# Kernel tuning notes

Measured on AMD Instinct MI355X. Metric: run time of the kernel, lower is better.

Reference implementation:

```python
import jax, jax.numpy as jnp
import numpy as np

N_NODES = 100_000
N_EDGES = 1_000_000
H = 128
NUM_STATES = 4
UPPER_T, LOWER_T, NUM_ITERS, TEMP_EVAL = 1.0, 0.1, 10000, 0.1


def temp_by_step(step, upper, lower, num_iters, temp_eval):
    # Python-level schedule: eval temp at step == -1, else linear anneal.
    if step == -1:
        return temp_eval
    frac = min(step / num_iters, 1.0)
    return upper + (lower - upper) * frac


def from_binary_states(states):
    # [*, k] bits -> integer id in [0, 2**k)
    weights = 2 ** jnp.arange(states.shape[-1])
    return (states * weights).sum(-1)


def setup_inputs() -> dict:
    key = jax.random.key(0)
    ks = jax.random.split(key, 20)
    N, E, h = N_NODES, N_EDGES, H
    node_states = jax.random.randint(ks[0], (N, NUM_STATES), 0, 2)
    edge_states = jax.random.randint(ks[1], (E, NUM_STATES), 0, 2)
    scalars = jax.random.normal(ks[2], (E, 1), jnp.float32)
    # first N edges are self-loops ordered by node id (required by the module's
    # node_scalars = scalars[src == dst] indexing convention)
    loops = jnp.arange(N)
    src = jax.random.randint(ks[3], (E - N,), 0, N)
    dst = jax.random.randint(ks[4], (E - N,), 0, N)
    dst = jnp.where(dst == src, (dst + 1) % N, dst)  # no accidental self-loops
    edge_index = jnp.stack([jnp.concatenate([loops, src]),
                            jnp.concatenate([loops, dst])])
    batched_reverse_idx = jax.random.randint(ks[5], (E,), 0, E)
    batch_scalars = jax.random.normal(ks[6], (E, 1, 1), jnp.float32)
    s = 0.02
    params = dict(
        node_emb=s * jax.random.normal(ks[7], (2 ** NUM_STATES, h), jnp.float32),
        edge_emb=s * jax.random.normal(ks[8], (2 ** NUM_STATES, h), jnp.float32),
        combine_W=s * jax.random.normal(ks[9], (2 * h, h), jnp.float32),
        combine_b=jnp.zeros((h,), jnp.float32),
        keep_W=s * jax.random.normal(ks[10], (h, 2), jnp.float32),
        keep_b=jnp.zeros((2,), jnp.float32),
        push_W=s * jax.random.normal(ks[11], (h, 2), jnp.float32),
        push_b=jnp.zeros((2,), jnp.float32),
        push_node_W=s * jax.random.normal(ks[12], (h, 2), jnp.float32),
        push_node_b=jnp.zeros((2,), jnp.float32),
        increment_W=s * jax.random.normal(ks[13], (h, 2), jnp.float32),
        increment_b=jnp.zeros((2,), jnp.float32),
    )
    return dict(node_states=node_states, edge_states=edge_states, scalars=scalars,
                edge_index=edge_index, batched_reverse_idx=batched_reverse_idx,
                batch_scalars=batch_scalars, processor_step=0, training_step=0,
                **params)


def reference(node_states, edge_states, scalars, edge_index, batched_reverse_idx,
              batch_scalars, processor_step, training_step,
              node_emb, edge_emb, combine_W, combine_b, keep_W, keep_b,
              push_W, push_b, push_node_W, push_node_b,
              increment_W, increment_b):
    N = node_states.shape[0]
    tau = temp_by_step(int(training_step), UPPER_T, LOWER_T, NUM_ITERS, TEMP_EVAL)
    # use_noise = config.use_noise (False) and training_step != -1 -> False

    node_fts = node_emb[from_binary_states(node_states)]   # [N, h]
    edge_fts = edge_emb[from_binary_states(edge_states)]   # [E, h]
    src, dst = edge_index[0], edge_index[1]
    fts = jnp.concatenate([edge_fts[batched_reverse_idx], node_fts[src]], axis=1)
    fts = fts @ combine_W + combine_b                       # [E, h]

    s = scalars.reshape(-1)                                 # [E]

    def pair_gumbel_first(W, b):
        # grouped (per-edge pair) softmax; take first component (== [::2])
        logits = (fts @ W + b) / tau                        # [E, 2]
        return jax.nn.softmax(logits, axis=-1)[:, 0]

    increment = 1.0 * pair_gumbel_first(increment_W, increment_b)
    keep = s * pair_gumbel_first(keep_W, keep_b)

    # push: first N edges are self-loops, self-loop of node i is edge i
    push_wo = pair_gumbel_first(push_W, push_b)
    push_w = pair_gumbel_first(push_node_W, push_node_b)
    node_scalars = s[:N]                                    # scalars at self-loops
    s_wo = s - node_scalars[dst]
    s_w = s_wo + node_scalars[src]
    acc = (jax.ops.segment_sum(push_wo * s_wo, dst, num_segments=N)
           + jax.ops.segment_sum(push_w * s_w, dst, num_segments=N))  # [N]
    edge_push = jnp.zeros_like(s).at[:N].set(acc)           # nonzero only on self-loops

    new_scalars = (increment + keep + edge_push)[:, None]   # [E, 1]
    target = batch_scalars[:, processor_step]               # [E, 1]
    loss = jnp.mean((target - new_scalars) ** 2)
    return new_scalars, loss
```

## Files before the change

### kernel.cpp

```cpp
#include <hip/hip_runtime.h>
#include <math.h>
#include <stdint.h>

#define N_NODES 100000
#define N_EDGES 1000000
#define N_NONLOOP (N_EDGES - N_NODES)
#define NXCD 8

typedef float  vfloat4 __attribute__((ext_vector_type(4)));
typedef int    vint4   __attribute__((ext_vector_type(4)));

#define XCC_ID_HWREG (20 | ((4 - 1) << 11))

__device__ __forceinline__ int get_xcc() {
    return __builtin_amdgcn_s_getreg(XCC_ID_HWREG) & (NXCD - 1);
}

__device__ __forceinline__ void l2_atomic_add(float* p, float v) {
    asm volatile("global_atomic_add_f32 %0, %1, off" :: "v"(p), "v"(v) : "memory");
}

__device__ __forceinline__ float get_invtau(const int* __restrict__ training_step) {
    int step = training_step[0];
    float tau;
    if (step == -1) {
        tau = 0.1f;
    } else {
        float frac = fminf((float)step / 10000.0f, 1.0f);
        tau = 1.0f + (0.1f - 1.0f) * frac;
    }
    return 1.0f / tau;
}

__device__ __forceinline__ float wave_reduce(float v) {
    #pragma unroll
    for (int off = 32; off > 0; off >>= 1) v += __shfl_down(v, off, 64);
    return v;
}

#define TAB_BLOCKS  132
#define NODE_BLOCKS 391
#define EI_BLOCKS   977

__global__ __launch_bounds__(256) void fused_pre(
    const int* __restrict__ node_states,
    const float* __restrict__ s,
    const int* __restrict__ edge_states,
    const int* __restrict__ brev,
    const float* __restrict__ node_emb,
    const float* __restrict__ edge_emb,
    const float* __restrict__ cW, const float* __restrict__ cb,
    const float* __restrict__ kW, const float* __restrict__ kb,
    const float* __restrict__ pW, const float* __restrict__ pb,
    const float* __restrict__ pnW, const float* __restrict__ pnb,
    const float* __restrict__ iW, const float* __restrict__ ib,
    const int* __restrict__ tstep,
    float2* __restrict__ node_pack,
    float* __restrict__ acc,
    uint8_t* __restrict__ ei,
    uint8_t* __restrict__ eib_node,
    float* __restrict__ tabs,
    float* __restrict__ lossp,
    float* __restrict__ loss_out,
    int ncopies)
{
    const int b = blockIdx.x;

    if (b < TAB_BLOCKS) {
        const int w    = b;
        const int lane = threadIdx.x & 63;
        const int wv   = threadIdx.x >> 6;
        const float invtau = get_invtau(tstep);
        __shared__ float part[4];

        float p = 0.f;
        if (w < 128) {
            const int isB = w >> 6, h = (w >> 4) & 3, i = w & 15;
            const float* emb = isB ? node_emb : edge_emb;
            const float* cWh = cW + isB * 128 * 128;
            float t0 = 0.f, t1 = 0.f;
            const int l0 = wv * 32;
            #pragma unroll 8
            for (int l = l0; l < l0 + 32; ++l) {
                const float el = emb[i * 128 + l];
                t0 += el * cWh[l * 128 + lane];
                t1 += el * cWh[l * 128 + 64 + lane];
            }
            const float* W = (h == 0) ? kW : (h == 1) ? pW : (h == 2) ? pnW : iW;
            const float wd0 = W[2 * lane] - W[2 * lane + 1];
            const float wd1 = W[2 * (lane + 64)] - W[2 * (lane + 64) + 1];
            p = t0 * wd0 + t1 * wd1;
        } else if (wv == 0) {
            const int h = w & 3;
            const float* W = (h == 0) ? kW : (h == 1) ? pW : (h == 2) ? pnW : iW;
            const float wd0 = W[2 * lane] - W[2 * lane + 1];
            const float wd1 = W[2 * (lane + 64)] - W[2 * (lane + 64) + 1];
            p = cb[lane] * wd0 + cb[64 + lane] * wd1;
        }
        p = wave_reduce(p);
        if (lane == 0) part[wv] = p;
        __syncthreads();
        if (threadIdx.x == 0) {
            const float tot = part[0] + part[1] + part[2] + part[3];
            if (w < 128) {
                const int isB = w >> 6, h = (w >> 4) & 3, i = w & 15;
                tabs[isB * 64 + i * 4 + h] = tot * invtau;
            } else {
                const int h = w & 3;
                const float* bb = (h == 0) ? kb : (h == 1) ? pb : (h == 2) ? pnb : ib;
                tabs[128 + h] = (tot + bb[0] - bb[1]) * invtau;
            }
        }
        return;
    }

    if (b < TAB_BLOCKS + NODE_BLOCKS) {
        const int n = (b - TAB_BLOCKS) * 256 + threadIdx.x;
        if (n < 256) lossp[n] = 0.f;
        if (n == 0) *loss_out = 0.f;
        if (n < N_NODES) {
            vint4 st = __builtin_nontemporal_load(&((const vint4*)node_states)[n]);
            const int idx = st.x + 2 * st.y + 4 * st.z + 8 * st.w;
            float2 np;
            np.x = s[n];
            np.y = __int_as_float(idx);
            node_pack[n] = np;
            for (int k = 0; k < ncopies; ++k) acc[(size_t)k * N_NODES + n] = 0.f;
            const int rev = brev[n];
            const int4 est = ((const int4*)edge_states)[rev];
            eib_node[n] = (uint8_t)(est.x + 2 * est.y + 4 * est.z + 8 * est.w);
        }
        return;
    }

    const int t = (b - TAB_BLOCKS - NODE_BLOCKS) * 256 + threadIdx.x;
    if (t < N_EDGES / 4) {
        const vint4* esp = (const vint4*)edge_states + 4 * t;
        vint4 e0 = __builtin_nontemporal_load(esp + 0);
        vint4 e1 = __builtin_nontemporal_load(esp + 1);
        vint4 e2 = __builtin_nontemporal_load(esp + 2);
        vint4 e3 = __builtin_nontemporal_load(esp + 3);
        const uint32_t i0 = e0.x + 2 * e0.y + 4 * e0.z + 8 * e0.w;
        const uint32_t i1 = e1.x + 2 * e1.y + 4 * e1.z + 8 * e1.w;
        const uint32_t i2 = e2.x + 2 * e2.y + 4 * e2.z + 8 * e2.w;
        const uint32_t i3 = e3.x + 2 * e3.y + 4 * e3.z + 8 * e3.w;
        ((uint32_t*)ei)[t] = i0 | (i1 << 8) | (i2 << 16) | (i3 << 24);
    }
}

template<int MODE>
__global__ __launch_bounds__(256) void edge_kernel(
    const float* __restrict__ s,
    const int* __restrict__ src,
    const int* __restrict__ dst,
    const int* __restrict__ brev,
    const uint8_t* __restrict__ ei,
    const float2* __restrict__ node_pack,
    const float* __restrict__ tabs,
    const float* __restrict__ target,
    float* __restrict__ acc,
    float* __restrict__ lossp,
    float* __restrict__ out,
    float* __restrict__ loss_out)
{
    __shared__ float4 sf[33];
    if (threadIdx.x < 33) sf[threadIdx.x] = ((const float4*)tabs)[threadIdx.x];
    __syncthreads();

    int xcc = 0;
    float* accx = acc;
    if (MODE == 1) {
        xcc  = get_xcc();
        accx = acc + (size_t)xcc * N_NODES;
    }

    const int t = blockIdx.x * blockDim.x + threadIdx.x;
    const bool active = (t < N_NONLOOP / 4);
    float lsum = 0.f;
    float ov[4], av[4];
    int   dsv[4];
    int   g = 0;

    if (active) {
        g = (N_NODES / 4) + t;
        const vint4   rv = __builtin_nontemporal_load(&((const vint4*)brev)[g]);
        const vint4   sr = __builtin_nontemporal_load(&((const vint4*)src)[g]);
        const vint4   ds = __builtin_nontemporal_load(&((const vint4*)dst)[g]);
        const vfloat4 sv = __builtin_nontemporal_load(&((const vfloat4*)s)[g]);
        const vfloat4 tg = __builtin_nontemporal_load(&((const vfloat4*)target)[g]);

        const int rvv[4] = {rv.x, rv.y, rv.z, rv.w};
        const int srv[4] = {sr.x, sr.y, sr.z, sr.w};
        dsv[0] = ds.x; dsv[1] = ds.y; dsv[2] = ds.z; dsv[3] = ds.w;
        const float svv[4] = {sv.x, sv.y, sv.z, sv.w};
        const float tgv[4] = {tg.x, tg.y, tg.z, tg.w};

        int    eidx[4];
        float2 np[4];
        float  sd[4];
        #pragma unroll
        for (int j = 0; j < 4; ++j) {
            eidx[j] = ei[rvv[j]];
            np[j]   = node_pack[srv[j]];
            sd[j]   = node_pack[dsv[j]].x;
        }

        const float4 c4 = sf[32];
        #pragma unroll
        for (int j = 0; j < 4; ++j) {
            const int   ni = __float_as_int(np[j].y);
            const float ss = np[j].x;
            const float4 a = sf[eidx[j]];
            const float4 b = sf[16 + ni];
            const float lk  = a.x + b.x + c4.x;
            const float lp  = a.y + b.y + c4.y;
            const float lpn = a.z + b.z + c4.z;
            const float li  = a.w + b.w + c4.w;
            const float pk  = 1.f / (1.f + __expf(-lk));
            const float pp  = 1.f / (1.f + __expf(-lp));
            const float ppn = 1.f / (1.f + __expf(-lpn));
            const float pi  = 1.f / (1.f + __expf(-li));

            const float s_wo = svv[j] - sd[j];
            const float s_w  = s_wo + ss;
            av[j] = pp * s_wo + ppn * s_w;

            ov[j] = pi + svv[j] * pk;
            const float d = tgv[j] - ov[j];
            lsum += d * d;
        }
    }

    lsum = wave_reduce(lsum);
    __shared__ float wsum[4];
    const int lane = threadIdx.x & 63, wid = threadIdx.x >> 6;
    if (lane == 0) wsum[wid] = lsum;
    __syncthreads();
    if (threadIdx.x == 0) {
        const float tot = (wsum[0] + wsum[1] + wsum[2] + wsum[3]) * (1.0f / (float)N_EDGES);
        if (MODE == 1) l2_atomic_add(&lossp[xcc * 32], tot);
        else           atomicAdd(loss_out, tot);
    }

    if (active) {
        #pragma unroll
        for (int j = 0; j < 4; ++j) {
            if (MODE == 1) l2_atomic_add(&accx[dsv[j]], av[j]);
            else           unsafeAtomicAdd(&acc[dsv[j]], av[j]);
        }
        vfloat4 o4 = {ov[0], ov[1], ov[2], ov[3]};
        __builtin_nontemporal_store(o4, &((vfloat4*)out)[g]);
    }
}

template<int NC>
__global__ __launch_bounds__(256) void finalize_nodes(
    const uint8_t* __restrict__ eib_node,
    const float2* __restrict__ node_pack,
    const float* __restrict__ tabs,
    const float* __restrict__ target,
    const float* __restrict__ acc,
    const float* __restrict__ lossp,
    float* __restrict__ out,
    float* __restrict__ loss_out)
{
    __shared__ float4 sf[33];
    if (threadIdx.x < 33) sf[threadIdx.x] = ((const float4*)tabs)[threadIdx.x];
    __syncthreads();

    const int n = blockIdx.x * blockDim.x + threadIdx.x;
    const bool active = (n < N_NODES);
    float sq = 0.f, v = 0.f;
    if (active) {
        const int    eidx = eib_node[n];
        const float2 np  = node_pack[n];
        const int    ni  = __float_as_int(np.y);
        const float  sv  = np.x;

        float a8 = 0.f;
        #pragma unroll
        for (int k = 0; k < NC; ++k) a8 += acc[(size_t)k * N_NODES + n];

        const float4 a  = sf[eidx];
        const float4 b  = sf[16 + ni];
        const float4 c4 = sf[32];
        const float lk  = a.x + b.x + c4.x;
        const float lpn = a.z + b.z + c4.z;
        const float li  = a.w + b.w + c4.w;
        const float pk  = 1.f / (1.f + __expf(-lk));
        const float ppn = 1.f / (1.f + __expf(-lpn));
        const float pi  = 1.f / (1.f + __expf(-li));

        v = pi + sv * (pk + ppn) + a8;
        const float d = target[n] - v;
        sq = d * d;
    }
    sq = wave_reduce(sq);
    __shared__ float wsum[4];
    const int lane = threadIdx.x & 63, wid = threadIdx.x >> 6;
    if (lane == 0) wsum[wid] = sq;
    __syncthreads();
    if (threadIdx.x == 0) {
        float tot = (wsum[0] + wsum[1] + wsum[2] + wsum[3]) * (1.0f / (float)N_EDGES);
        if (blockIdx.x == 0) {
            #pragma unroll
            for (int k = 0; k < NXCD; ++k) tot += lossp[k * 32];
        }
        atomicAdd(loss_out, tot);
    }
    if (active) out[n] = v;
}

extern "C" void kernel_launch(void* const* d_in, const int* in_sizes, int n_in,
                              void* d_out, int out_size, void* d_ws, size_t ws_size,
                              hipStream_t stream) {
    const int*   node_states   = (const int*)d_in[0];
    const int*   edge_states   = (const int*)d_in[1];
    const float* scalars       = (const float*)d_in[2];
    const int*   edge_index    = (const int*)d_in[3];
    const int*   brev          = (const int*)d_in[4];
    const float* batch_scalars = (const float*)d_in[5];
    const int*   training_step = (const int*)d_in[7];
    const float* node_emb  = (const float*)d_in[8];
    const float* edge_emb  = (const float*)d_in[9];
    const float* combine_W = (const float*)d_in[10];
    const float* combine_b = (const float*)d_in[11];
    const float* keep_W  = (const float*)d_in[12];
    const float* keep_b  = (const float*)d_in[13];
    const float* push_W  = (const float*)d_in[14];
    const float* push_b  = (const float*)d_in[15];
    const float* pushn_W = (const float*)d_in[16];
    const float* pushn_b = (const float*)d_in[17];
    const float* inc_W   = (const float*)d_in[18];
    const float* inc_b   = (const float*)d_in[19];

    float* out = (float*)d_out;

    const size_t need_scoped = 2048 + (size_t)NXCD * N_NODES * 4 + (size_t)N_NODES * 8
                             + N_EDGES + N_NODES + 1024;
    const bool scoped = (ws_size >= need_scoped);
    const int nc = scoped ? NXCD : 1;

    char* ws = (char*)d_ws;
    float*   tabs      = (float*)ws;
    float*   lossp     = (float*)(ws + 1024);
    float*   acc       = (float*)(ws + 2048);
    float2*  node_pack = (float2*)(ws + 2048 + (size_t)nc * N_NODES * 4);
    uint8_t* ei        = (uint8_t*)node_pack + (size_t)N_NODES * 8;
    uint8_t* eib_node  = ei + N_EDGES;

    const int* srcp = edge_index;
    const int* dstp = edge_index + N_EDGES;

    fused_pre<<<TAB_BLOCKS + NODE_BLOCKS + EI_BLOCKS, 256, 0, stream>>>(
        node_states, scalars, edge_states, brev, node_emb, edge_emb,
        combine_W, combine_b, keep_W, keep_b, push_W, push_b,
        pushn_W, pushn_b, inc_W, inc_b, training_step,
        node_pack, acc, ei, eib_node, tabs, lossp, out + N_EDGES, nc);

    const int ethreads = N_NONLOOP / 4;
    const int eblocks  = (ethreads + 255) / 256;
    if (scoped) {
        edge_kernel<1><<<eblocks, 256, 0, stream>>>(
            scalars, srcp, dstp, brev, ei, node_pack, tabs, batch_scalars,
            acc, lossp, out, out + N_EDGES);
        finalize_nodes<NXCD><<<(N_NODES + 255) / 256, 256, 0, stream>>>(
            eib_node, node_pack, tabs, batch_scalars, acc, lossp, out, out + N_EDGES);
    } else {
        edge_kernel<0><<<eblocks, 256, 0, stream>>>(
            scalars, srcp, dstp, brev, ei, node_pack, tabs, batch_scalars,
            acc, lossp, out, out + N_EDGES);
        finalize_nodes<1><<<(N_NODES + 255) / 256, 256, 0, stream>>>(
            eib_node, node_pack, tabs, batch_scalars, acc, lossp, out, out + N_EDGES);
    }
}
```

Before: 180.0 us.

## Use fixed-point integer atomics and drop packed node buffer

Scatter-add of per-edge push values now uses integer atomics on values scaled by 2^20, converted back to float in the node finalize kernel. The precomputed node_pack and per-node edge-state bytes are removed; the edge kernel gathers scalars and a byte node-state index directly, and finalize looks up edge indices via brev. This cuts preprocessing writes and gather width and may make atomics cheaper, at the risk of fixed-point precision loss or overflow.

Result: faster. 174.6 us (-3.0%).

```diff
diff --git a/kernel.cpp b/kernel.cpp
--- a/kernel.cpp
+++ b/kernel.cpp
@@ -7,6 +7,9 @@
 #define N_NONLOOP (N_EDGES - N_NODES)
 #define NXCD 8
 
+#define ACC_SCALE   1048576.0f
+#define ACC_INV     (1.0f / 1048576.0f)
+
 typedef float  vfloat4 __attribute__((ext_vector_type(4)));
 typedef int    vint4   __attribute__((ext_vector_type(4)));
 
@@ -16,7 +19,10 @@
     return __builtin_amdgcn_s_getreg(XCC_ID_HWREG) & (NXCD - 1);
 }
 
-__device__ __forceinline__ void l2_atomic_add(float* p, float v) {
+__device__ __forceinline__ void l2_atomic_add_u32(uint32_t* p, uint32_t v) {
+    asm volatile("global_atomic_add %0, %1, off" :: "v"(p), "v"(v) : "memory");
+}
+__device__ __forceinline__ void l2_atomic_add_f32(float* p, float v) {
     asm volatile("global_atomic_add_f32 %0, %1, off" :: "v"(p), "v"(v) : "memory");
 }
 
@@ -44,9 +50,7 @@
 
 __global__ __launch_bounds__(256) void fused_pre(
     const int* __restrict__ node_states,
-    const float* __restrict__ s,
     const int* __restrict__ edge_states,
-    const int* __restrict__ brev,
     const float* __restrict__ node_emb,
     const float* __restrict__ edge_emb,
     const float* __restrict__ cW, const float* __restrict__ cb,
@@ -55,10 +59,9 @@
     const float* __restrict__ pnW, const float* __restrict__ pnb,
     const float* __restrict__ iW, const float* __restrict__ ib,
     const int* __restrict__ tstep,
-    float2* __restrict__ node_pack,
-    float* __restrict__ acc,
+    uint32_t* __restrict__ acc,
     uint8_t* __restrict__ ei,
-    uint8_t* __restrict__ eib_node,
+    uint8_t* __restrict__ nib,
     float* __restrict__ tabs,
     float* __restrict__ lossp,
     float* __restrict__ loss_out,
@@ -120,15 +123,8 @@
         if (n == 0) *loss_out = 0.f;
         if (n < N_NODES) {
             vint4 st = __builtin_nontemporal_load(&((const vint4*)node_states)[n]);
-            const int idx = st.x + 2 * st.y + 4 * st.z + 8 * st.w;
-            float2 np;
-            np.x = s[n];
-            np.y = __int_as_float(idx);
-            node_pack[n] = np;
-            for (int k = 0; k < ncopies; ++k) acc[(size_t)k * N_NODES + n] = 0.f;
-            const int rev = brev[n];
-            const int4 est = ((const int4*)edge_states)[rev];
-            eib_node[n] = (uint8_t)(est.x + 2 * est.y + 4 * est.z + 8 * est.w);
+            nib[n] = (uint8_t)(st.x + 2 * st.y + 4 * st.z + 8 * st.w);
+            for (int k = 0; k < ncopies; ++k) acc[(size_t)k * N_NODES + n] = 0u;
         }
         return;
     }
@@ -155,20 +151,20 @@
     const int* __restrict__ dst,
     const int* __restrict__ brev,
     const uint8_t* __restrict__ ei,
-    const float2* __restrict__ node_pack,
+    const uint8_t* __restrict__ nib,
     const float* __restrict__ tabs,
     const float* __restrict__ target,
-    float* __restrict__ acc,
+    uint32_t* __restrict__ acc,
     float* __restrict__ lossp,
     float* __restrict__ out,
     float* __restrict__ loss_out)
 {
-    __shared__ float4 sf[33];
+    __shared__ float4 sf[MODE ? 160 : 33];
     if (threadIdx.x < 33) sf[threadIdx.x] = ((const float4*)tabs)[threadIdx.x];
     __syncthreads();
 
     int xcc = 0;
-    float* accx = acc;
+    uint32_t* accx = acc;
     if (MODE == 1) {
         xcc  = get_xcc();
         accx = acc + (size_t)xcc * N_NODES;
@@ -177,7 +173,8 @@
     const int t = blockIdx.x * blockDim.x + threadIdx.x;
     const bool active = (t < N_NONLOOP / 4);
     float lsum = 0.f;
-    float ov[4], av[4];
+    float ov[4];
+    int   iv[4];
     int   dsv[4];
     int   g = 0;
 
@@ -195,23 +192,21 @@
         const float svv[4] = {sv.x, sv.y, sv.z, sv.w};
         const float tgv[4] = {tg.x, tg.y, tg.z, tg.w};
 
-        int    eidx[4];
-        float2 np[4];
-        float  sd[4];
+        int   eidx[4], ni[4];
+        float ss[4], sd[4];
         #pragma unroll
         for (int j = 0; j < 4; ++j) {
             eidx[j] = ei[rvv[j]];
-            np[j]   = node_pack[srv[j]];
-            sd[j]   = node_pack[dsv[j]].x;
+            ni[j]   = nib[srv[j]];
+            ss[j]   = s[srv[j]];
+            sd[j]   = s[dsv[j]];
         }
 
         const float4 c4 = sf[32];
         #pragma unroll
         for (int j = 0; j < 4; ++j) {
-            const int   ni = __float_as_int(np[j].y);
-            const float ss = np[j].x;
             const float4 a = sf[eidx[j]];
-            const float4 b = sf[16 + ni];
+            const float4 b = sf[16 + ni[j]];
             const float lk  = a.x + b.x + c4.x;
             const float lp  = a.y + b.y + c4.y;
             const float lpn = a.z + b.z + c4.z;
@@ -222,8 +217,8 @@
             const float pi  = 1.f / (1.f + __expf(-li));
 
             const float s_wo = svv[j] - sd[j];
-            const float s_w  = s_wo + ss;
-            av[j] = pp * s_wo + ppn * s_w;
+            const float s_w  = s_wo + ss[j];
+            iv[j] = __float2int_rn((pp * s_wo + ppn * s_w) * ACC_SCALE);
 
             ov[j] = pi + svv[j] * pk;
             const float d = tgv[j] - ov[j];
@@ -238,15 +233,15 @@
     __syncthreads();
     if (threadIdx.x == 0) {
         const float tot = (wsum[0] + wsum[1] + wsum[2] + wsum[3]) * (1.0f / (float)N_EDGES);
-        if (MODE == 1) l2_atomic_add(&lossp[xcc * 32], tot);
+        if (MODE == 1) l2_atomic_add_f32(&lossp[xcc * 32], tot);
         else           atomicAdd(loss_out, tot);
     }
 
     if (active) {
         #pragma unroll
         for (int j = 0; j < 4; ++j) {
-            if (MODE == 1) l2_atomic_add(&accx[dsv[j]], av[j]);
-            else           unsafeAtomicAdd(&acc[dsv[j]], av[j]);
+            if (MODE == 1) l2_atomic_add_u32(&accx[dsv[j]], (uint32_t)iv[j]);
+            else           atomicAdd((unsigned int*)&acc[dsv[j]], (unsigned int)iv[j]);
         }
         vfloat4 o4 = {ov[0], ov[1], ov[2], ov[3]};
         __builtin_nontemporal_store(o4, &((vfloat4*)out)[g]);
@@ -255,11 +250,13 @@
 
 template<int NC>
 __global__ __launch_bounds__(256) void finalize_nodes(
-    const uint8_t* __restrict__ eib_node,
-    const float2* __restrict__ node_pack,
+    const float* __restrict__ s,
+    const int* __restrict__ brev,
+    const uint8_t* __restrict__ ei,
+    const uint8_t* __restrict__ nib,
     const float* __restrict__ tabs,
     const float* __restrict__ target,
-    const float* __restrict__ acc,
+    const uint32_t* __restrict__ acc,
     const float* __restrict__ lossp,
     float* __restrict__ out,
     float* __restrict__ loss_out)
@@ -272,14 +269,14 @@
     const bool active = (n < N_NODES);
     float sq = 0.f, v = 0.f;
     if (active) {
-        const int    eidx = eib_node[n];
-        const float2 np  = node_pack[n];
-        const int    ni  = __float_as_int(np.y);
-        const float  sv  = np.x;
-
-        float a8 = 0.f;
+        const int  eidx = ei[brev[n]];
+        const int  ni   = nib[n];
+        const float sv  = s[n];
+
+        uint32_t asum = 0u;
         #pragma unroll
-        for (int k = 0; k < NC; ++k) a8 += acc[(size_t)k * N_NODES + n];
+        for (int k = 0; k < NC; ++k) asum += acc[(size_t)k * N_NODES + n];
+        const float a8 = (float)(int)asum * ACC_INV;
 
         const float4 a  = sf[eidx];
         const float4 b  = sf[16 + ni];
@@ -336,41 +333,39 @@
 
     float* out = (float*)d_out;
 
-    const size_t need_scoped = 2048 + (size_t)NXCD * N_NODES * 4 + (size_t)N_NODES * 8
-                             + N_EDGES + N_NODES + 1024;
+    const size_t need_scoped = 2048 + (size_t)NXCD * N_NODES * 4 + N_EDGES + N_NODES;
     const bool scoped = (ws_size >= need_scoped);
     const int nc = scoped ? NXCD : 1;
 
     char* ws = (char*)d_ws;
-    float*   tabs      = (float*)ws;
-    float*   lossp     = (float*)(ws + 1024);
-    float*   acc       = (float*)(ws + 2048);
-    float2*  node_pack = (float2*)(ws + 2048 + (size_t)nc * N_NODES * 4);
-    uint8_t* ei        = (uint8_t*)node_pack + (size_t)N_NODES * 8;
-    uint8_t* eib_node  = ei + N_EDGES;
+    float*    tabs  = (float*)ws;
+    float*    lossp = (float*)(ws + 1024);
+    uint32_t* acc   = (uint32_t*)(ws + 2048);
+    uint8_t*  ei    = (uint8_t*)(ws + 2048 + (size_t)nc * N_NODES * 4);
+    uint8_t*  nib   = ei + N_EDGES;
 
     const int* srcp = edge_index;
     const int* dstp = edge_index + N_EDGES;
 
     fused_pre<<<TAB_BLOCKS + NODE_BLOCKS + EI_BLOCKS, 256, 0, stream>>>(
-        node_states, scalars, edge_states, brev, node_emb, edge_emb,
+        node_states, edge_states, node_emb, edge_emb,
         combine_W, combine_b, keep_W, keep_b, push_W, push_b,
         pushn_W, pushn_b, inc_W, inc_b, training_step,
-        node_pack, acc, ei, eib_node, tabs, lossp, out + N_EDGES, nc);
+        acc, ei, nib, tabs, lossp, out + N_EDGES, nc);
 
     const int ethreads = N_NONLOOP / 4;
     const int eblocks  = (ethreads + 255) / 256;
     if (scoped) {
         edge_kernel<1><<<eblocks, 256, 0, stream>>>(
-            scalars, srcp, dstp, brev, ei, node_pack, tabs, batch_scalars,
+            scalars, srcp, dstp, brev, ei, nib, tabs, batch_scalars,
             acc, lossp, out, out + N_EDGES);
         finalize_nodes<NXCD><<<(N_NODES + 255) / 256, 256, 0, stream>>>(
-            eib_node, node_pack, tabs, batch_scalars, acc, lossp, out, out + N_EDGES);
+            scalars, brev, ei, nib, tabs, batch_scalars, acc, lossp, out, out + N_EDGES);
     } else {
         edge_kernel<0><<<eblocks, 256, 0, stream>>>(
-            scalars, srcp, dstp, brev, ei, node_pack, tabs, batch_scalars,
+            scalars, srcp, dstp, brev, ei, nib, tabs, batch_scalars,
             acc, lossp, out, out + N_EDGES);
         finalize_nodes<1><<<(N_NODES + 255) / 256, 256, 0, stream>>>(
-            eib_node, node_pack, tabs, batch_scalars, acc, lossp, out, out + N_EDGES);
-    }
-}
+            scalars, brev, ei, nib, tabs, batch_scalars, acc, lossp, out, out + N_EDGES);
+    }
+}
```
